# Optimization experiments

Measured on AMD Instinct MI355X. Metric: run time of the kernel, lower is better.

The kernel has to match this reference:

```python
import jax, jax.numpy as jnp
import numpy as np

B, H, W, C = 128, 8, 32, 512
RNN = 512; EMB = 512; ATT = 512
VOCAB = 110          # vocab_size -> classes = VOCAB + 1
MAXLEN = 30          # loop runs MAXLEN + 1 steps


def setup_inputs() -> dict:
    key = jax.random.key(0)
    ks = jax.random.split(key, 16)
    w = lambda i, shape: jax.random.normal(ks[i], shape, jnp.float32) * 0.02
    return {
        "features": jax.random.normal(ks[0], (B, H, W, C), jnp.float32),
        "holistic": jax.random.normal(ks[1], (B, RNN), jnp.float32),
        "gt": jax.random.randint(ks[2], (B, MAXLEN + 1), 0, VOCAB + 1),
        "embed_W": w(3, (VOCAB + 1, EMB)),
        "k0": w(4, (EMB, 4 * RNN)), "rk0": w(5, (RNN, 4 * RNN)), "b0": jnp.zeros((4 * RNN,), jnp.float32),
        "k1": w(6, (RNN, 4 * RNN)), "rk1": w(7, (RNN, 4 * RNN)), "b1": jnp.zeros((4 * RNN,), jnp.float32),
        "Wh": w(8, (RNN, ATT)),                       # 1x1 conv on (B,1,1,RNN) == dense
        "Wf": w(9, (3, 3, C, ATT)), "bf": jnp.zeros((ATT,), jnp.float32),
        "wa": w(10, (ATT, 1)),                        # 1x1 conv -> scalar attention logit
        "out_W": w(11, (2 * RNN, VOCAB + 1)), "out_b": jnp.zeros((VOCAB + 1,), jnp.float32),
    }


def _lstm(x, h, c, k, rk, b):
    # Keras LSTMCell: gates order i, f, g(cell), o
    z = x @ k + h @ rk + b
    i, f, g, o = jnp.split(z, 4, axis=-1)
    c2 = jax.nn.sigmoid(f) * c + jax.nn.sigmoid(i) * jnp.tanh(g)
    h2 = jax.nn.sigmoid(o) * jnp.tanh(c2)
    return h2, c2


def reference(features, holistic, gt, embed_W, k0, rk0, b0, k1, rk1, b1,
              Wh, Wf, bf, wa, out_W, out_b):
    Bb, Hh, Ww, Cc = features.shape
    # features_projector (3x3 conv, SAME) is timestep-invariant: precompute once
    fproj = jax.lax.conv_general_dilated(
        features, Wf, (1, 1), "SAME",
        dimension_numbers=("NHWC", "HWIO", "NHWC")) + bf          # (B,H,W,ATT)

    zeros = jnp.zeros((Bb, RNN), features.dtype)
    # prime stacked LSTM with holistic vector (zero initial state)
    h0, c0 = _lstm(holistic, zeros, zeros, k0, rk0, b0)
    h1, c1 = _lstm(h0, zeros, zeros, k1, rk1, b1)

    # teacher forcing: step 0 uses SOS token = vocab_size+1 (out-of-range -> zero one-hot),
    # step t>0 uses gt[:, t-1]
    sos = jnp.full((1, Bb), VOCAB + 1, gt.dtype)
    symbols = jnp.concatenate([sos, gt[:, :MAXLEN].T], axis=0)     # (T, B), T = MAXLEN+1

    def step(carry, sym):
        h0, c0, h1, c1 = carry
        x = jax.nn.one_hot(sym, VOCAB + 1, dtype=features.dtype) @ embed_W   # (B, EMB)
        h0, c0 = _lstm(x, h0, c0, k0, rk0, b0)
        h1, c1 = _lstm(h0, h1, c1, k1, rk1, b1)
        # attention over conv feature map
        hp = h1 @ Wh                                               # (B, ATT)
        proj = jnp.tanh(fproj + hp[:, None, None, :])              # (B,H,W,ATT)
        att = (proj @ wa).reshape(Bb, Hh * Ww)                     # (B, H*W)
        att = jax.nn.softmax(att, axis=-1).reshape(Bb, Hh, Ww, 1)
        glimpse = jnp.sum(features * att, axis=(1, 2))             # (B, C)
        logits = jnp.concatenate([h1, glimpse], axis=-1) @ out_W + out_b
        return (h0, c0, h1, c1), logits

    _, logits = jax.lax.scan(step, (h0, c0, h1, c1), symbols)      # (T, B, VOCAB+1)
    return jnp.transpose(logits, (1, 0, 2))                        # (B, T, VOCAB+1)
```

## Files before the change

### kernel.cpp

```cpp
#include <hip/hip_runtime.h>


typedef __bf16 bf16;
typedef bf16 bf16x8 __attribute__((ext_vector_type(8)));
typedef float f32x4 __attribute__((ext_vector_type(4)));

#define MFMA16(a, b, c) __builtin_amdgcn_mfma_f32_16x16x32_bf16((a), (b), (c), 0, 0, 0)

__device__ __forceinline__ float b2f(unsigned short u) {
    return __uint_as_float(((unsigned int)u) << 16);
}
__device__ __forceinline__ unsigned short f2b(float f) {
    unsigned int x = __float_as_uint(f);
    unsigned int r = (x + 0x7fffu + ((x >> 16) & 1u)) >> 16;
    return (unsigned short)r;
}
__device__ __forceinline__ float exp2_raw(float x) {
    float r;
    asm("v_exp_f32 %0, %1" : "=v"(r) : "v"(x));
    return r;
}
__device__ __forceinline__ float tanh_fast(float x) {
    const float e = exp2_raw(2.885390082f * x);
    return 1.0f - 2.0f * __builtin_amdgcn_rcpf(e + 1.0f);
}
__device__ __forceinline__ float sig_fast(float x) {
    return __builtin_amdgcn_rcpf(1.0f + exp2_raw(-1.44269504f * x));
}
__device__ __forceinline__ void gl16(const ushort* g, ushort* l) {
    __builtin_amdgcn_global_load_lds(
        (const __attribute__((address_space(1))) void*)g,
        (__attribute__((address_space(3))) void*)l, 16, 0, 0);
}

__global__ void detect_dtype(const void* __restrict__ feat, int* __restrict__ flag) {
    if (threadIdx.x == 0 && blockIdx.x == 0) {
        const ushort* u = (const ushort*)feat;
        int cnt = 0;
        for (int i = 0; i < 128; i += 2) {
            const int e = (u[i] >> 7) & 0xFF;
            if (e >= 96 && e <= 150) ++cnt;
        }
        *flag = (cnt >= 40) ? 0 : 1;
    }
}

__global__ __launch_bounds__(256) void cvt_bf16(
    const void* __restrict__ src, ushort* __restrict__ dst, int n,
    const int* __restrict__ flag) {
    const int i = blockIdx.x * 256 + threadIdx.x;
    if (i >= n) return;
    if (*flag) dst[i] = f2b(((const float*)src)[i]);
    else       dst[i] = ((const ushort*)src)[i];
}

__global__ __launch_bounds__(256) void cvt_f32(
    const void* __restrict__ src, float* __restrict__ dst, int n,
    const int* __restrict__ flag) {
    const int i = blockIdx.x * 256 + threadIdx.x;
    if (i >= n) return;
    if (*flag) dst[i] = ((const float*)src)[i];
    else       dst[i] = b2f(((const ushort*)src)[i]);
}

__global__ __launch_bounds__(256) void build_featpad(
    const void* __restrict__ feat, ushort* __restrict__ featPad,
    const int* __restrict__ flag) {
    const int i = blockIdx.x * 256 + threadIdx.x;
    if (i >= 128 * 10 * 34 * 512) return;
    const int c = i & 511;
    const int xy = i >> 9;
    const int x = xy % 34;
    const int t2 = xy / 34;
    const int y = t2 % 10;
    const int b = t2 / 10;
    ushort v = 0;
    if (y >= 1 && y <= 8 && x >= 1 && x <= 32) {
        const size_t si = ((size_t)((b * 8 + y - 1) * 32 + (x - 1)) << 9) + c;
        v = *flag ? f2b(((const float*)feat)[si]) : ((const ushort*)feat)[si];
    }
    featPad[i] = v;
}

__global__ __launch_bounds__(256) void transpose_any(
    const void* __restrict__ in, ushort* __restrict__ out, int R, int C,
    const int* __restrict__ flag) {
    __shared__ float s[32][33];
    const int f32 = *flag;
    const int nbc = C >> 5;
    const int rb = blockIdx.x / nbc, cb = blockIdx.x % nbc;
    const int tx = threadIdx.x & 31, ty = threadIdx.x >> 5;
#pragma unroll
    for (int k = 0; k < 4; ++k) {
        const size_t idx = (size_t)(rb * 32 + ty + k * 8) * C + cb * 32 + tx;
        s[ty + k * 8][tx] = f32 ? ((const float*)in)[idx] : b2f(((const ushort*)in)[idx]);
    }
    __syncthreads();
#pragma unroll
    for (int k = 0; k < 4; ++k)
        out[(size_t)(cb * 32 + ty + k * 8) * R + rb * 32 + tx] = f2b(s[tx][ty + k * 8]);
}

__global__ __launch_bounds__(256) void woT_build(
    const float* __restrict__ outWf, ushort* __restrict__ WoTpad) {
    const int i = blockIdx.x * 256 + threadIdx.x;
    if (i >= 131072) return;
    const int v = i >> 10, k = i & 1023;
    WoTpad[i] = (v < 111) ? f2b(outWf[k * 111 + v]) : (ushort)0;
}

__global__ __launch_bounds__(256) void conv_fproj(
    const ushort* __restrict__ featPad, const ushort* __restrict__ WfT,
    const float* __restrict__ bff, ushort* __restrict__ fproj) {
    __shared__ __align__(16) ushort As[128 * 64];
    __shared__ __align__(16) ushort Bs[128 * 64];
    const int tid = threadIdx.x;
    const int nb = blockIdx.x >> 8;
    const int rb = blockIdx.x & 255;
    const int b = rb >> 1, p0 = (rb & 1) << 7;
    const int w = tid >> 6, lane = tid & 63, l15 = lane & 15, q = lane >> 4;
    const int wr = (w >> 1) << 6, wc = (w & 1) << 6;
    const int chunkoff = (((lane & 7) ^ (lane >> 3)) << 3);
    int aoff[4], boff[4];
#pragma unroll
    for (int i = 0; i < 4; ++i) {
        const int r = w * 32 + (lane >> 3) + i * 8;
        const int p = p0 + r;
        const int yy = p >> 5, xx = p & 31;
        aoff[i] = (((b * 10 + yy) * 34 + xx) << 9) + chunkoff;
        boff[i] = (nb * 128 + r) * 4608 + chunkoff;
    }
    const int swa = l15 & 7;
    f32x4 acc[4][4] = {};
    for (int kb = 0; kb < 72; ++kb) {
        const int tap = kb >> 3;
        const int dy = tap / 3, dx = tap - dy * 3;
        const int koffA = ((dy * 34 + dx) << 9) + ((kb & 7) << 6);
        const int koffB = kb * 64;
        __syncthreads();
#pragma unroll
        for (int i = 0; i < 4; ++i) {
            gl16(featPad + aoff[i] + koffA, &As[(w * 32 + i * 8) * 64]);
            gl16(WfT + boff[i] + koffB, &Bs[(w * 32 + i * 8) * 64]);
        }
        __syncthreads();
#pragma unroll
        for (int ks = 0; ks < 64; ks += 32) {
            const int cq = (ks >> 3) + q;
            const int col = ((cq ^ swa) << 3);
            bf16x8 af[4], bfr[4];
#pragma unroll
            for (int i = 0; i < 4; ++i) af[i] = *(const bf16x8*)&As[(wr + i * 16 + l15) * 64 + col];
#pragma unroll
            for (int j = 0; j < 4; ++j) bfr[j] = *(const bf16x8*)&Bs[(wc + j * 16 + l15) * 64 + col];
#pragma unroll
            for (int i = 0; i < 4; ++i)
#pragma unroll
                for (int j = 0; j < 4; ++j)
                    acc[i][j] = MFMA16(af[i], bfr[j], acc[i][j]);
        }
    }
    const int rowbase = rb * 128 + wr, colbase = nb * 128 + wc;
#pragma unroll
    for (int i = 0; i < 4; ++i)
#pragma unroll
        for (int j = 0; j < 4; ++j)
#pragma unroll
            for (int rr = 0; rr < 4; ++rr) {
                const int row = rowbase + i * 16 + q * 4 + rr;
                const int col = colbase + j * 16 + l15;
                fproj[(size_t)row * 512 + col] = f2b(acc[i][j][rr] + bff[col]);
            }
}

__global__ __launch_bounds__(256) void gemm_bt(
    const ushort* __restrict__ A, const ushort* __restrict__ BT,
    float* __restrict__ C, int M, int N, int K, int lda) {
    __shared__ __align__(16) bf16 As[128][72];
    __shared__ __align__(16) bf16 Bs[128][72];
    const int tid = threadIdx.x;
    const int nnb = N >> 7;
    const int rb = blockIdx.x / nnb, nb = blockIdx.x % nnb;
    const int ar = tid >> 1, ah = (tid & 1) << 5;
    const int w = tid >> 6, lane = tid & 63, l15 = lane & 15, q = lane >> 4;
    const int wr = (w >> 1) << 6, wc = (w & 1) << 6;
    const int r_glob = rb * 128 + ar;
    const bool aval = (r_glob < M);
    const int r_ld = aval ? r_glob : 0;
    f32x4 acc[4][4] = {};
    const int nkb = K >> 6;
    for (int kb = 0; kb < nkb; ++kb) {
        const uint4 z4 = {0u, 0u, 0u, 0u};
        const uint4* asrc = (const uint4*)(A + (size_t)r_ld * lda + kb * 64 + ah);
        uint4 a0 = asrc[0], a1 = asrc[1], a2 = asrc[2], a3 = asrc[3];
        if (!aval) { a0 = z4; a1 = z4; a2 = z4; a3 = z4; }
        const uint4* bsrc = (const uint4*)(BT + (size_t)(nb * 128 + ar) * K + kb * 64 + ah);
        uint4 b0v = bsrc[0], b1v = bsrc[1], b2v = bsrc[2], b3v = bsrc[3];
        __syncthreads();
        *(uint4*)&As[ar][ah] = a0;
        *(uint4*)&As[ar][ah + 8] = a1;
        *(uint4*)&As[ar][ah + 16] = a2;
        *(uint4*)&As[ar][ah + 24] = a3;
        *(uint4*)&Bs[ar][ah] = b0v;
        *(uint4*)&Bs[ar][ah + 8] = b1v;
        *(uint4*)&Bs[ar][ah + 16] = b2v;
        *(uint4*)&Bs[ar][ah + 24] = b3v;
        __syncthreads();
#pragma unroll
        for (int ks = 0; ks < 64; ks += 32) {
            bf16x8 af[4], bfr[4];
#pragma unroll
            for (int i = 0; i < 4; ++i) af[i] = *(const bf16x8*)&As[wr + i * 16 + l15][ks + q * 8];
#pragma unroll
            for (int j = 0; j < 4; ++j) bfr[j] = *(const bf16x8*)&Bs[wc + j * 16 + l15][ks + q * 8];
#pragma unroll
            for (int i = 0; i < 4; ++i)
#pragma unroll
                for (int j = 0; j < 4; ++j)
                    acc[i][j] = MFMA16(af[i], bfr[j], acc[i][j]);
        }
    }
#pragma unroll
    for (int i = 0; i < 4; ++i)
#pragma unroll
        for (int j = 0; j < 4; ++j)
#pragma unroll
            for (int rr = 0; rr < 4; ++rr) {
                const int row = rb * 128 + wr + i * 16 + q * 4 + rr;
                const int col = nb * 128 + wc + j * 16 + l15;
                if (row < M) C[(size_t)row * N + col] = acc[i][j][rr];
            }
}

__global__ __launch_bounds__(256) void lstm_stage(
    int t,
    const ushort* __restrict__ holistic, const int* __restrict__ gt,
    const float* __restrict__ b0f, const float* __restrict__ b1f,
    const ushort* __restrict__ k0T, const ushort* __restrict__ rk0T,
    const ushort* __restrict__ k1T, const ushort* __restrict__ rk1T,
    const float* __restrict__ E0,
    ushort* h0b0, ushort* h0b1, ushort* h1b0, ushort* h1b1,
    float* c0buf, float* c1buf, ushort* HG) {
    const int part = blockIdx.x >> 7;
    const int bi = blockIdx.x & 127;
    const ushort *A1 = nullptr, *A2 = nullptr, *B1 = nullptr, *B2 = nullptr;
    const float* bias = nullptr;
    ushort *hout = nullptr, *hout2 = nullptr;
    float* cbuf = nullptr;
    bool useC = false, useE = false;
    if (part == 0) {
        if (!(t == -2 || (t >= 0 && t <= 30))) return;
        bias = b0f; cbuf = c0buf;
        if (t == -2) { A1 = holistic; B1 = k0T; hout = h0b1; }
        else {
            A1 = ((t + 1) & 1) ? h0b1 : h0b0;
            B1 = rk0T;
            hout = (t & 1) ? h0b1 : h0b0;
            useC = true; useE = true;
        }
    } else {
        if (!(t == -1 || (t >= 1 && t <= 31))) return;
        bias = b1f; cbuf = c1buf;
        if (t == -1) { A1 = h0b1; B1 = k1T; hout = h1b1; }
        else {
            const int s = t - 1;
            A1 = (s & 1) ? h0b1 : h0b0;
            A2 = ((s + 1) & 1) ? h1b1 : h1b0;
            B1 = k1T; B2 = rk1T;
            hout = (s & 1) ? h1b1 : h1b0;
            hout2 = HG + (size_t)s * 131072;
            useC = true;
        }
    }
    const int m0 = (bi >> 5) << 5;
    const int cc0 = (bi & 31) << 4;
    const int tid = threadIdx.x;
    const int w = tid >> 6, lane = tid & 63, l15 = lane & 15, q = lane >> 4;
    __shared__ __align__(16) ushort As1[32 * 520];
    __shared__ __align__(16) ushort As2[32 * 520];
    __shared__ float zs[4][32][17];
#pragma unroll
    for (int it = 0; it < 8; ++it) {
        const int idx = tid + it * 256;
        const int row = idx >> 6, chv = idx & 63;
        *(uint4*)&As1[row * 520 + chv * 8] =
            *(const uint4*)(A1 + (size_t)(m0 + row) * 512 + chv * 8);
    }
    if (A2) {
#pragma unroll
        for (int it = 0; it < 8; ++it) {
            const int idx = tid + it * 256;
            const int row = idx >> 6, chv = idx & 63;
            *(uint4*)&As2[row * 520 + chv * 8] =
                *(const uint4*)(A2 + (size_t)(m0 + row) * 512 + chv * 8);
        }
    }
    __syncthreads();
    const int nkb = A2 ? 16 : 8;
    const size_t brow = (size_t)(w * 512 + cc0 + l15) * 512 + q * 8;
    auto bp = [&](int kb) -> const ushort* {
        const ushort* base = (kb < 8) ? B1 : B2;
        return base + brow + (kb & 7) * 64;
    };
    bf16x8 b0a = *(const bf16x8*)bp(0), b1a = *(const bf16x8*)(bp(0) + 32);
    bf16x8 b0b = *(const bf16x8*)bp(1), b1b = *(const bf16x8*)(bp(1) + 32);
    bf16x8 b0c = *(const bf16x8*)bp(2), b1c = *(const bf16x8*)(bp(2) + 32);
    f32x4 acc0 = {}, acc1 = {};
    for (int kb = 0; kb < nkb; ++kb) {
        const bf16x8 p0 = b0a, p1 = b1a;
        b0a = b0b; b1a = b1b; b0b = b0c; b1b = b1c;
        if (kb + 3 < nkb) {
            b0c = *(const bf16x8*)bp(kb + 3);
            b1c = *(const bf16x8*)(bp(kb + 3) + 32);
        }
        const ushort* asrc = (kb < 8) ? As1 : As2;
        const int kk = (kb & 7) * 64 + q * 8;
        bf16x8 a00 = *(const bf16x8*)&asrc[l15 * 520 + kk];
        bf16x8 a10 = *(const bf16x8*)&asrc[(16 + l15) * 520 + kk];
        bf16x8 a01 = *(const bf16x8*)&asrc[l15 * 520 + kk + 32];
        bf16x8 a11 = *(const bf16x8*)&asrc[(16 + l15) * 520 + kk + 32];
        acc0 = MFMA16(a00, p0, acc0);
        acc1 = MFMA16(a10, p0, acc1);
        acc0 = MFMA16(a01, p1, acc0);
        acc1 = MFMA16(a11, p1, acc1);
    }
#pragma unroll
    for (int rr = 0; rr < 4; ++rr) {
        zs[w][q * 4 + rr][l15] = acc0[rr];
        zs[w][16 + q * 4 + rr][l15] = acc1[rr];
    }
    __syncthreads();
#pragma unroll
    for (int it = 0; it < 2; ++it) {
        const int e = tid + it * 256;
        const int mm = e >> 4, cc = e & 15;
        const int brow2 = m0 + mm, col = cc0 + cc;
        float zi = zs[0][mm][cc] + bias[col];
        float zf = zs[1][mm][cc] + bias[512 + col];
        float zg = zs[2][mm][cc] + bias[1024 + col];
        float zo = zs[3][mm][cc] + bias[1536 + col];
        if (useE) {
            const int s = (t == 0) ? 111 : gt[brow2 * 31 + t - 1];
            if (s >= 0 && s < 111) {
                const float* er = E0 + (size_t)s * 2048;
                zi += er[col]; zf += er[512 + col]; zg += er[1024 + col]; zo += er[1536 + col];
            }
        }
        const float cp = useC ? cbuf[brow2 * 512 + col] : 0.0f;
        const float c2 = sig_fast(zf) * cp + sig_fast(zi) * tanh_fast(zg);
        const float h = sig_fast(zo) * tanh_fast(c2);
        cbuf[brow2 * 512 + col] = c2;
        hout[brow2 * 512 + col] = f2b(h);
        if (hout2) hout2[brow2 * 1024 + col] = f2b(h);
    }
}

__global__ __launch_bounds__(256) void att_logits(
    const ushort* __restrict__ fproj, const float* __restrict__ HP,
    const float* __restrict__ waf, float* __restrict__ attL) {
    __shared__ float hpS[16][512];
    __shared__ float waS[512];
    __shared__ float accS[128][17];
    const int tid = threadIdx.x;
    const int b = blockIdx.x >> 2, ph = (blockIdx.x >> 1) & 1, th = blockIdx.x & 1;
    const int t0 = th << 4, tc = th ? 15 : 16;
    const int pl = tid & 127, ch = tid >> 7;
    const int p = ph * 128 + pl;
    for (int i = tid; i < 16 * 512; i += 256) {
        const int tt = i >> 9, c = i & 511;
        hpS[tt][c] = (tt < tc) ? 2.885390082f * HP[((size_t)(t0 + tt) * 128 + b) * 512 + c] : 0.0f;
    }
    waS[tid] = -2.0f * waf[tid];
    if (tid < 256) waS[256 + tid] = -2.0f * waf[256 + tid];
    __syncthreads();
    float sumW = 0.f;
    {
        const float* wh = &waS[ch * 256];
        for (int c4 = 0; c4 < 64; ++c4) {
            const float4 wv = *(const float4*)&wh[c4 * 4];
            sumW += wv.x + wv.y + wv.z + wv.w;
        }
        sumW *= -0.5f;
    }
    float acc[16];
#pragma unroll
    for (int tt = 0; tt < 16; ++tt) acc[tt] = 0.f;
    const ushort* frow = fproj + (size_t)(b * 256 + p) * 512 + ch * 256;
    for (int c8 = 0; c8 < 32; ++c8) {
        const int cc = ch * 256 + c8 * 8;
        const uint4 fv = *(const uint4*)(frow + c8 * 8);
        float f[8];
        f[0] = b2f((unsigned short)(fv.x & 0xffff)); f[1] = b2f((unsigned short)(fv.x >> 16));
        f[2] = b2f((unsigned short)(fv.y & 0xffff)); f[3] = b2f((unsigned short)(fv.y >> 16));
        f[4] = b2f((unsigned short)(fv.z & 0xffff)); f[5] = b2f((unsigned short)(fv.z >> 16));
        f[6] = b2f((unsigned short)(fv.w & 0xffff)); f[7] = b2f((unsigned short)(fv.w >> 16));
#pragma unroll
        for (int j = 0; j < 8; ++j) f[j] *= 2.885390082f;
        const float4 w0 = *(const float4*)&waS[cc];
        const float4 w1 = *(const float4*)&waS[cc + 4];
#pragma unroll
        for (int tt = 0; tt < 16; ++tt) {
            const float4 h0 = *(const float4*)&hpS[tt][cc];
            const float4 h1 = *(const float4*)&hpS[tt][cc + 4];
            float s = acc[tt];
            s = fmaf(__builtin_amdgcn_rcpf(exp2_raw(f[0] + h0.x) + 1.0f), w0.x, s);
            s = fmaf(__builtin_amdgcn_rcpf(exp2_raw(f[1] + h0.y) + 1.0f), w0.y, s);
            s = fmaf(__builtin_amdgcn_rcpf(exp2_raw(f[2] + h0.z) + 1.0f), w0.z, s);
            s = fmaf(__builtin_amdgcn_rcpf(exp2_raw(f[3] + h0.w) + 1.0f), w0.w, s);
            s = fmaf(__builtin_amdgcn_rcpf(exp2_raw(f[4] + h1.x) + 1.0f), w1.x, s);
            s = fmaf(__builtin_amdgcn_rcpf(exp2_raw(f[5] + h1.y) + 1.0f), w1.y, s);
            s = fmaf(__builtin_amdgcn_rcpf(exp2_raw(f[6] + h1.z) + 1.0f), w1.z, s);
            s = fmaf(__builtin_amdgcn_rcpf(exp2_raw(f[7] + h1.w) + 1.0f), w1.w, s);
            acc[tt] = s;
        }
    }
    if (ch == 1) {
#pragma unroll
        for (int tt = 0; tt < 16; ++tt) accS[pl][tt] = acc[tt] + sumW;
    }
    __syncthreads();
    if (ch == 0) {
        for (int tt = 0; tt < tc; ++tt)
            attL[((size_t)(t0 + tt) * 128 + b) * 256 + p] = acc[tt] + sumW + accS[pl][tt];
    }
}

__global__ __launch_bounds__(256) void glimpse_kernel(
    const ushort* __restrict__ featPad, const float* __restrict__ attL,
    ushort* __restrict__ HG) {
    __shared__ __align__(16) float attT[256 * 36];
    const int tid = threadIdx.x;
    const int b = blockIdx.x >> 1, chh = blockIdx.x & 1;
    const int c0 = chh << 8;
    const int w = tid >> 6, lane = tid & 63;
    for (int i = tid; i < 31 * 256; i += 256) {
        const int tt = i >> 8, p = i & 255;
        attT[p * 36 + tt] = attL[((size_t)tt * 128 + b) * 256 + p];
    }
    __syncthreads();
    for (int tt = w; tt < 31; tt += 4) {
        float v0 = attT[lane * 36 + tt], v1 = attT[(lane + 64) * 36 + tt];
        float v2 = attT[(lane + 128) * 36 + tt], v3 = attT[(lane + 192) * 36 + tt];
        float mx = fmaxf(fmaxf(v0, v1), fmaxf(v2, v3));
#pragma unroll
        for (int m = 1; m < 64; m <<= 1) mx = fmaxf(mx, __shfl_xor(mx, m));
        const float e0 = exp2_raw((v0 - mx) * 1.44269504f);
        const float e1 = exp2_raw((v1 - mx) * 1.44269504f);
        const float e2 = exp2_raw((v2 - mx) * 1.44269504f);
        const float e3 = exp2_raw((v3 - mx) * 1.44269504f);
        float s = e0 + e1 + e2 + e3;
#pragma unroll
        for (int m = 1; m < 64; m <<= 1) s += __shfl_xor(s, m);
        const float r = 1.0f / s;
        attT[lane * 36 + tt] = e0 * r;  attT[(lane + 64) * 36 + tt] = e1 * r;
        attT[(lane + 128) * 36 + tt] = e2 * r;  attT[(lane + 192) * 36 + tt] = e3 * r;
    }
    __syncthreads();
    float acc[31];
#pragma unroll
    for (int tt = 0; tt < 31; ++tt) acc[tt] = 0.f;
    for (int p = 0; p < 256; ++p) {
        const size_t fi = (((size_t)(b * 10 + (p >> 5) + 1) * 34 + (p & 31) + 1) << 9) + c0 + tid;
        const float fv = b2f(featPad[fi]);
        const float4 a0 = *(const float4*)&attT[p * 36];
        const float4 a1 = *(const float4*)&attT[p * 36 + 4];
        const float4 a2 = *(const float4*)&attT[p * 36 + 8];
        const float4 a3 = *(const float4*)&attT[p * 36 + 12];
        const float4 a4 = *(const float4*)&attT[p * 36 + 16];
        const float4 a5 = *(const float4*)&attT[p * 36 + 20];
        const float4 a6 = *(const float4*)&attT[p * 36 + 24];
        const float4 a7 = *(const float4*)&attT[p * 36 + 28];
        acc[0] = fmaf(fv, a0.x, acc[0]);   acc[1] = fmaf(fv, a0.y, acc[1]);
        acc[2] = fmaf(fv, a0.z, acc[2]);   acc[3] = fmaf(fv, a0.w, acc[3]);
        acc[4] = fmaf(fv, a1.x, acc[4]);   acc[5] = fmaf(fv, a1.y, acc[5]);
        acc[6] = fmaf(fv, a1.z, acc[6]);   acc[7] = fmaf(fv, a1.w, acc[7]);
        acc[8] = fmaf(fv, a2.x, acc[8]);   acc[9] = fmaf(fv, a2.y, acc[9]);
        acc[10] = fmaf(fv, a2.z, acc[10]); acc[11] = fmaf(fv, a2.w, acc[11]);
        acc[12] = fmaf(fv, a3.x, acc[12]); acc[13] = fmaf(fv, a3.y, acc[13]);
        acc[14] = fmaf(fv, a3.z, acc[14]); acc[15] = fmaf(fv, a3.w, acc[15]);
        acc[16] = fmaf(fv, a4.x, acc[16]); acc[17] = fmaf(fv, a4.y, acc[17]);
        acc[18] = fmaf(fv, a4.z, acc[18]); acc[19] = fmaf(fv, a4.w, acc[19]);
        acc[20] = fmaf(fv, a5.x, acc[20]); acc[21] = fmaf(fv, a5.y, acc[21]);
        acc[22] = fmaf(fv, a5.z, acc[22]); acc[23] = fmaf(fv, a5.w, acc[23]);
        acc[24] = fmaf(fv, a6.x, acc[24]); acc[25] = fmaf(fv, a6.y, acc[25]);
        acc[26] = fmaf(fv, a6.z, acc[26]); acc[27] = fmaf(fv, a6.w, acc[27]);
        acc[28] = fmaf(fv, a7.x, acc[28]); acc[29] = fmaf(fv, a7.y, acc[29]);
        acc[30] = fmaf(fv, a7.z, acc[30]);
    }
#pragma unroll
    for (int tt = 0; tt < 31; ++tt)
        HG[((size_t)tt * 128 + b) * 1024 + 512 + c0 + tid] = f2b(acc[tt]);
}

__global__ __launch_bounds__(256) void logits_store(
    const float* __restrict__ C, const float* __restrict__ outBf,
    void* __restrict__ out, const int* __restrict__ flag) {
    const int i = blockIdx.x * 256 + threadIdx.x;
    if (i >= 3968 * 111) return;
    const int r = i / 111, v = i - r * 111;
    const int tt = r >> 7, b = r & 127;
    const float a = C[(size_t)r * 128 + v] + outBf[v];
    const size_t oi = ((size_t)b * 31 + tt) * 111 + v;
    if (*flag) ((float*)out)[oi] = a;
    else       ((ushort*)out)[oi] = f2b(a);
}

extern "C" void kernel_launch(void* const* d_in, const int* in_sizes, int n_in,
                              void* d_out, int out_size, void* d_ws, size_t ws_size,
                              hipStream_t stream) {
    (void)in_sizes; (void)n_in; (void)out_size;
    const void* features = d_in[0];
    const void* holistic = d_in[1];
    const int*  gt       = (const int*)d_in[2];
    const void* embed_W  = d_in[3];
    const void* k0 = d_in[4];
    const void* rk0 = d_in[5];
    const void* b0 = d_in[6];
    const void* k1 = d_in[7];
    const void* rk1 = d_in[8];
    const void* b1 = d_in[9];
    const void* Wh = d_in[10];
    const void* Wf = d_in[11];
    const void* bfv = d_in[12];
    const void* wa = d_in[13];
    const void* outW = d_in[14];
    const void* outB = d_in[15];

    char* ws = (char*)d_ws;
    size_t off = 0;
    auto take = [&](size_t bytes) -> char* {
        char* p = ws + off;
        off += (bytes + 255) & ~(size_t)255;
        return p;
    };
    int*    flag    = (int*)take(256);
    ushort* featPad = (ushort*)take(128ull * 10 * 34 * 512 * 2);
    ushort* holB  = (ushort*)take(65536ull * 2);
    ushort* embB  = (ushort*)take(56832ull * 2);
    float*  b0f   = (float*)take(2048ull * 4);
    float*  b1f   = (float*)take(2048ull * 4);
    float*  bff   = (float*)take(512ull * 4);
    float*  waf   = (float*)take(512ull * 4);
    float*  outBf = (float*)take(111ull * 4);
    float*  outWf = (float*)take(113664ull * 4);
    ushort* fproj = (ushort*)take(32768ull * 512 * 2);
    ushort* WfT   = (ushort*)take(4608ull * 512 * 2);
    ushort* k0T   = (ushort*)take(2048ull * 512 * 2);
    ushort* rk0T  = (ushort*)take(2048ull * 512 * 2);
    ushort* k1T   = (ushort*)take(2048ull * 512 * 2);
    ushort* rk1T  = (ushort*)take(2048ull * 512 * 2);
    ushort* WhT   = (ushort*)take(512ull * 512 * 2);
    float*  E0    = (float*)take(111ull * 2048 * 4);
    ushort* h0b0  = (ushort*)take(128ull * 512 * 2);
    ushort* h0b1  = (ushort*)take(128ull * 512 * 2);
    ushort* h1b0  = (ushort*)take(128ull * 512 * 2);
    ushort* h1b1  = (ushort*)take(128ull * 512 * 2);
    float*  c0buf = (float*)take(128ull * 512 * 4);
    float*  c1buf = (float*)take(128ull * 512 * 4);
    ushort* HG    = (ushort*)take(3968ull * 1024 * 2);
    float*  HP    = (float*)take(3968ull * 512 * 4);
    float*  attL  = (float*)take(31ull * 128 * 256 * 4);
    float*  Cout   = (float*)attL;
    ushort* WoTpad = (ushort*)((char*)attL + 3968ull * 128 * 4);
    if (off > ws_size) return;

    detect_dtype<<<dim3(1), dim3(64), 0, stream>>>(features, flag);
    build_featpad<<<dim3(87040), dim3(256), 0, stream>>>(features, featPad, flag);
    cvt_bf16<<<dim3(256), dim3(256), 0, stream>>>(holistic, holB, 65536, flag);
    cvt_bf16<<<dim3(222), dim3(256), 0, stream>>>(embed_W, embB, 56832, flag);
    cvt_f32<<<dim3(8), dim3(256), 0, stream>>>(b0, b0f, 2048, flag);
    cvt_f32<<<dim3(8), dim3(256), 0, stream>>>(b1, b1f, 2048, flag);
    cvt_f32<<<dim3(2), dim3(256), 0, stream>>>(bfv, bff, 512, flag);
    cvt_f32<<<dim3(2), dim3(256), 0, stream>>>(wa, waf, 512, flag);
    cvt_f32<<<dim3(1), dim3(256), 0, stream>>>(outB, outBf, 111, flag);
    cvt_f32<<<dim3(444), dim3(256), 0, stream>>>(outW, outWf, 113664, flag);
    transpose_any<<<dim3(16 * 64), dim3(256), 0, stream>>>(k0, k0T, 512, 2048, flag);
    transpose_any<<<dim3(16 * 64), dim3(256), 0, stream>>>(rk0, rk0T, 512, 2048, flag);
    transpose_any<<<dim3(16 * 64), dim3(256), 0, stream>>>(k1, k1T, 512, 2048, flag);
    transpose_any<<<dim3(16 * 64), dim3(256), 0, stream>>>(rk1, rk1T, 512, 2048, flag);
    transpose_any<<<dim3(16 * 16), dim3(256), 0, stream>>>(Wh, WhT, 512, 512, flag);
    transpose_any<<<dim3(144 * 16), dim3(256), 0, stream>>>(Wf, WfT, 4608, 512, flag);
    conv_fproj<<<dim3(1024), dim3(256), 0, stream>>>(featPad, WfT, bff, fproj);
    gemm_bt<<<dim3(16), dim3(256), 0, stream>>>(embB, k0T, E0, 111, 2048, 512, 512);
    for (int t = -2; t <= 31; ++t)
        lstm_stage<<<dim3(256), dim3(256), 0, stream>>>(t, holB, gt, b0f, b1f,
            k0T, rk0T, k1T, rk1T, E0, h0b0, h0b1, h1b0, h1b1, c0buf, c1buf, HG);
    gemm_bt<<<dim3(31 * 4), dim3(256), 0, stream>>>(HG, WhT, HP, 3968, 512, 512, 1024);
    att_logits<<<dim3(512), dim3(256), 0, stream>>>(fproj, HP, waf, attL);
    glimpse_kernel<<<dim3(256), dim3(256), 0, stream>>>(featPad, attL, HG);
    woT_build<<<dim3(512), dim3(256), 0, stream>>>(outWf, WoTpad);
    gemm_bt<<<dim3(31), dim3(256), 0, stream>>>(HG, WoTpad, Cout, 3968, 128, 1024, 1024);
    logits_store<<<dim3(1721), dim3(256), 0, stream>>>(Cout, outBf, d_out, flag);
}
```

Before: 933.4 us.

## Fuse conv projection and LSTM steps into one persistent kernel with grid barriers

Replaces the 34 per-timestep LSTM launches with one persistent kernel whose 256 LSTM blocks loop over timesteps and sync through atomic counters acting as grid barriers. The same launch also carries the 1024 conv_fproj blocks, so the timestep-invariant conv can run alongside the serial LSTM chain instead of before it. This removes launch overhead and overlaps the conv with the recurrence. It relies on all 256 LSTM blocks being co-resident and risks deadlock or slowdown if conv blocks take the CUs first. Sharing one large shared-memory buffer may also lower occupancy for the conv blocks.

```diff
diff --git a/kernel.cpp b/kernel.cpp
--- a/kernel.cpp
+++ b/kernel.cpp
@@ -43,6 +43,10 @@
         }
         *flag = (cnt >= 40) ? 0 : 1;
     }
+}
+
+__global__ void zero_cnt(int* __restrict__ cnt) {
+    if (threadIdx.x < 64) cnt[threadIdx.x] = 0;
 }
 
 __global__ __launch_bounds__(256) void cvt_bf16(
@@ -107,70 +111,6 @@
     if (i >= 131072) return;
     const int v = i >> 10, k = i & 1023;
     WoTpad[i] = (v < 111) ? f2b(outWf[k * 111 + v]) : (ushort)0;
-}
-
-__global__ __launch_bounds__(256) void conv_fproj(
-    const ushort* __restrict__ featPad, const ushort* __restrict__ WfT,
-    const float* __restrict__ bff, ushort* __restrict__ fproj) {
-    __shared__ __align__(16) ushort As[128 * 64];
-    __shared__ __align__(16) ushort Bs[128 * 64];
-    const int tid = threadIdx.x;
-    const int nb = blockIdx.x >> 8;
-    const int rb = blockIdx.x & 255;
-    const int b = rb >> 1, p0 = (rb & 1) << 7;
-    const int w = tid >> 6, lane = tid & 63, l15 = lane & 15, q = lane >> 4;
-    const int wr = (w >> 1) << 6, wc = (w & 1) << 6;
-    const int chunkoff = (((lane & 7) ^ (lane >> 3)) << 3);
-    int aoff[4], boff[4];
-#pragma unroll
-    for (int i = 0; i < 4; ++i) {
-        const int r = w * 32 + (lane >> 3) + i * 8;
-        const int p = p0 + r;
-        const int yy = p >> 5, xx = p & 31;
-        aoff[i] = (((b * 10 + yy) * 34 + xx) << 9) + chunkoff;
-        boff[i] = (nb * 128 + r) * 4608 + chunkoff;
-    }
-    const int swa = l15 & 7;
-    f32x4 acc[4][4] = {};
-    for (int kb = 0; kb < 72; ++kb) {
-        const int tap = kb >> 3;
-        const int dy = tap / 3, dx = tap - dy * 3;
-        const int koffA = ((dy * 34 + dx) << 9) + ((kb & 7) << 6);
-        const int koffB = kb * 64;
-        __syncthreads();
-#pragma unroll
-        for (int i = 0; i < 4; ++i) {
-            gl16(featPad + aoff[i] + koffA, &As[(w * 32 + i * 8) * 64]);
-            gl16(WfT + boff[i] + koffB, &Bs[(w * 32 + i * 8) * 64]);
-        }
-        __syncthreads();
-#pragma unroll
-        for (int ks = 0; ks < 64; ks += 32) {
-            const int cq = (ks >> 3) + q;
-            const int col = ((cq ^ swa) << 3);
-            bf16x8 af[4], bfr[4];
-#pragma unroll
-            for (int i = 0; i < 4; ++i) af[i] = *(const bf16x8*)&As[(wr + i * 16 + l15) * 64 + col];
-#pragma unroll
-            for (int j = 0; j < 4; ++j) bfr[j] = *(const bf16x8*)&Bs[(wc + j * 16 + l15) * 64 + col];
-#pragma unroll
-            for (int i = 0; i < 4; ++i)
-#pragma unroll
-                for (int j = 0; j < 4; ++j)
-                    acc[i][j] = MFMA16(af[i], bfr[j], acc[i][j]);
-        }
-    }
-    const int rowbase = rb * 128 + wr, colbase = nb * 128 + wc;
-#pragma unroll
-    for (int i = 0; i < 4; ++i)
-#pragma unroll
-        for (int j = 0; j < 4; ++j)
-#pragma unroll
-            for (int rr = 0; rr < 4; ++rr) {
-                const int row = rowbase + i * 16 + q * 4 + rr;
-                const int col = colbase + j * 16 + l15;
-                fproj[(size_t)row * 512 + col] = f2b(acc[i][j][rr] + bff[col]);
-            }
 }
 
 __global__ __launch_bounds__(256) void gemm_bt(
@@ -232,126 +172,213 @@
             }
 }
 
-__global__ __launch_bounds__(256) void lstm_stage(
-    int t,
+__global__ __launch_bounds__(256) void conv_lstm_mega(
+    const ushort* __restrict__ featPad, const ushort* __restrict__ WfT,
+    const float* __restrict__ bff, ushort* __restrict__ fproj,
     const ushort* __restrict__ holistic, const int* __restrict__ gt,
     const float* __restrict__ b0f, const float* __restrict__ b1f,
     const ushort* __restrict__ k0T, const ushort* __restrict__ rk0T,
     const ushort* __restrict__ k1T, const ushort* __restrict__ rk1T,
     const float* __restrict__ E0,
     ushort* h0b0, ushort* h0b1, ushort* h1b0, ushort* h1b1,
-    float* c0buf, float* c1buf, ushort* HG) {
+    float* c0buf, float* c1buf, ushort* HG, int* cnt) {
+    __shared__ __align__(16) ushort smem[37632];
+    const int tid = threadIdx.x;
+    const int w = tid >> 6, lane = tid & 63, l15 = lane & 15, q = lane >> 4;
+
+    if (blockIdx.x >= 256) {
+        ushort* As = smem;
+        ushort* Bs = smem + 8192;
+        const int cidx = blockIdx.x - 256;
+        const int nb = cidx >> 8;
+        const int rb = cidx & 255;
+        const int b = rb >> 1, p0 = (rb & 1) << 7;
+        const int wr = (w >> 1) << 6, wc = (w & 1) << 6;
+        const int chunkoff = (((lane & 7) ^ (lane >> 3)) << 3);
+        int aoff[4], boff[4];
+#pragma unroll
+        for (int i = 0; i < 4; ++i) {
+            const int r = w * 32 + (lane >> 3) + i * 8;
+            const int p = p0 + r;
+            const int yy = p >> 5, xx = p & 31;
+            aoff[i] = (((b * 10 + yy) * 34 + xx) << 9) + chunkoff;
+            boff[i] = (nb * 128 + r) * 4608 + chunkoff;
+        }
+        const int swa = l15 & 7;
+        f32x4 acc[4][4] = {};
+        for (int kb = 0; kb < 72; ++kb) {
+            const int tap = kb >> 3;
+            const int dy = tap / 3, dx = tap - dy * 3;
+            const int koffA = ((dy * 34 + dx) << 9) + ((kb & 7) << 6);
+            const int koffB = kb * 64;
+            __syncthreads();
+#pragma unroll
+            for (int i = 0; i < 4; ++i) {
+                gl16(featPad + aoff[i] + koffA, &As[(w * 32 + i * 8) * 64]);
+                gl16(WfT + boff[i] + koffB, &Bs[(w * 32 + i * 8) * 64]);
+            }
+            __syncthreads();
+#pragma unroll
+            for (int ks = 0; ks < 64; ks += 32) {
+                const int cq = (ks >> 3) + q;
+                const int col = ((cq ^ swa) << 3);
+                bf16x8 af[4], bfr[4];
+#pragma unroll
+                for (int i = 0; i < 4; ++i) af[i] = *(const bf16x8*)&As[(wr + i * 16 + l15) * 64 + col];
+#pragma unroll
+                for (int j = 0; j < 4; ++j) bfr[j] = *(const bf16x8*)&Bs[(wc + j * 16 + l15) * 64 + col];
+#pragma unroll
+                for (int i = 0; i < 4; ++i)
+#pragma unroll
+                    for (int j = 0; j < 4; ++j)
+                        acc[i][j] = MFMA16(af[i], bfr[j], acc[i][j]);
+            }
+        }
+        const int rowbase = rb * 128 + wr, colbase = nb * 128 + wc;
+#pragma unroll
+        for (int i = 0; i < 4; ++i)
+#pragma unroll
+            for (int j = 0; j < 4; ++j)
+#pragma unroll
+                for (int rr = 0; rr < 4; ++rr) {
+                    const int row = rowbase + i * 16 + q * 4 + rr;
+                    const int col = colbase + j * 16 + l15;
+                    fproj[(size_t)row * 512 + col] = f2b(acc[i][j][rr] + bff[col]);
+                }
+        return;
+    }
+
+    ushort* As1 = smem;
+    ushort* As2 = smem + 16640;
+    float*  zsf = (float*)(smem + 33280);
     const int part = blockIdx.x >> 7;
     const int bi = blockIdx.x & 127;
-    const ushort *A1 = nullptr, *A2 = nullptr, *B1 = nullptr, *B2 = nullptr;
-    const float* bias = nullptr;
-    ushort *hout = nullptr, *hout2 = nullptr;
-    float* cbuf = nullptr;
-    bool useC = false, useE = false;
-    if (part == 0) {
-        if (!(t == -2 || (t >= 0 && t <= 30))) return;
-        bias = b0f; cbuf = c0buf;
-        if (t == -2) { A1 = holistic; B1 = k0T; hout = h0b1; }
-        else {
-            A1 = ((t + 1) & 1) ? h0b1 : h0b0;
-            B1 = rk0T;
-            hout = (t & 1) ? h0b1 : h0b0;
-            useC = true; useE = true;
-        }
-    } else {
-        if (!(t == -1 || (t >= 1 && t <= 31))) return;
-        bias = b1f; cbuf = c1buf;
-        if (t == -1) { A1 = h0b1; B1 = k1T; hout = h1b1; }
-        else {
-            const int s = t - 1;
-            A1 = (s & 1) ? h0b1 : h0b0;
-            A2 = ((s + 1) & 1) ? h1b1 : h1b0;
-            B1 = k1T; B2 = rk1T;
-            hout = (s & 1) ? h1b1 : h1b0;
-            hout2 = HG + (size_t)s * 131072;
-            useC = true;
-        }
-    }
     const int m0 = (bi >> 5) << 5;
     const int cc0 = (bi & 31) << 4;
-    const int tid = threadIdx.x;
-    const int w = tid >> 6, lane = tid & 63, l15 = lane & 15, q = lane >> 4;
-    __shared__ __align__(16) ushort As1[32 * 520];
-    __shared__ __align__(16) ushort As2[32 * 520];
-    __shared__ float zs[4][32][17];
-#pragma unroll
-    for (int it = 0; it < 8; ++it) {
-        const int idx = tid + it * 256;
-        const int row = idx >> 6, chv = idx & 63;
-        *(uint4*)&As1[row * 520 + chv * 8] =
-            *(const uint4*)(A1 + (size_t)(m0 + row) * 512 + chv * 8);
-    }
-    if (A2) {
-#pragma unroll
-        for (int it = 0; it < 8; ++it) {
-            const int idx = tid + it * 256;
-            const int row = idx >> 6, chv = idx & 63;
-            *(uint4*)&As2[row * 520 + chv * 8] =
-                *(const uint4*)(A2 + (size_t)(m0 + row) * 512 + chv * 8);
-        }
-    }
-    __syncthreads();
-    const int nkb = A2 ? 16 : 8;
-    const size_t brow = (size_t)(w * 512 + cc0 + l15) * 512 + q * 8;
-    auto bp = [&](int kb) -> const ushort* {
-        const ushort* base = (kb < 8) ? B1 : B2;
-        return base + brow + (kb & 7) * 64;
-    };
-    bf16x8 b0a = *(const bf16x8*)bp(0), b1a = *(const bf16x8*)(bp(0) + 32);
-    bf16x8 b0b = *(const bf16x8*)bp(1), b1b = *(const bf16x8*)(bp(1) + 32);
-    bf16x8 b0c = *(const bf16x8*)bp(2), b1c = *(const bf16x8*)(bp(2) + 32);
-    f32x4 acc0 = {}, acc1 = {};
-    for (int kb = 0; kb < nkb; ++kb) {
-        const bf16x8 p0 = b0a, p1 = b1a;
-        b0a = b0b; b1a = b1b; b0b = b0c; b1b = b1c;
-        if (kb + 3 < nkb) {
-            b0c = *(const bf16x8*)bp(kb + 3);
-            b1c = *(const bf16x8*)(bp(kb + 3) + 32);
-        }
-        const ushort* asrc = (kb < 8) ? As1 : As2;
-        const int kk = (kb & 7) * 64 + q * 8;
-        bf16x8 a00 = *(const bf16x8*)&asrc[l15 * 520 + kk];
-        bf16x8 a10 = *(const bf16x8*)&asrc[(16 + l15) * 520 + kk];
-        bf16x8 a01 = *(const bf16x8*)&asrc[l15 * 520 + kk + 32];
-        bf16x8 a11 = *(const bf16x8*)&asrc[(16 + l15) * 520 + kk + 32];
-        acc0 = MFMA16(a00, p0, acc0);
-        acc1 = MFMA16(a10, p0, acc1);
-        acc0 = MFMA16(a01, p1, acc0);
-        acc1 = MFMA16(a11, p1, acc1);
-    }
-#pragma unroll
-    for (int rr = 0; rr < 4; ++rr) {
-        zs[w][q * 4 + rr][l15] = acc0[rr];
-        zs[w][16 + q * 4 + rr][l15] = acc1[rr];
-    }
-    __syncthreads();
-#pragma unroll
-    for (int it = 0; it < 2; ++it) {
-        const int e = tid + it * 256;
-        const int mm = e >> 4, cc = e & 15;
-        const int brow2 = m0 + mm, col = cc0 + cc;
-        float zi = zs[0][mm][cc] + bias[col];
-        float zf = zs[1][mm][cc] + bias[512 + col];
-        float zg = zs[2][mm][cc] + bias[1024 + col];
-        float zo = zs[3][mm][cc] + bias[1536 + col];
-        if (useE) {
-            const int s = (t == 0) ? 111 : gt[brow2 * 31 + t - 1];
-            if (s >= 0 && s < 111) {
-                const float* er = E0 + (size_t)s * 2048;
-                zi += er[col]; zf += er[512 + col]; zg += er[1024 + col]; zo += er[1536 + col];
-            }
-        }
-        const float cp = useC ? cbuf[brow2 * 512 + col] : 0.0f;
-        const float c2 = sig_fast(zf) * cp + sig_fast(zi) * tanh_fast(zg);
-        const float h = sig_fast(zo) * tanh_fast(c2);
-        cbuf[brow2 * 512 + col] = c2;
-        hout[brow2 * 512 + col] = f2b(h);
-        if (hout2) hout2[brow2 * 1024 + col] = f2b(h);
+
+    for (int t = -2; t <= 31; ++t) {
+        const int k = t + 2;
+        if (k > 0) {
+            if (tid == 0) {
+                while (__hip_atomic_load(&cnt[k - 1], __ATOMIC_RELAXED,
+                                         __HIP_MEMORY_SCOPE_AGENT) < 256)
+                    __builtin_amdgcn_s_sleep(1);
+            }
+            __syncthreads();
+            __threadfence();
+        }
+        const ushort *A1 = nullptr, *A2 = nullptr, *B1 = nullptr, *B2 = nullptr;
+        const float* bias = nullptr;
+        ushort *hout = nullptr, *hout2 = nullptr;
+        float* cbuf = nullptr;
+        bool useC = false, useE = false, active = false;
+        if (part == 0) {
+            if (t == -2 || (t >= 0 && t <= 30)) {
+                active = true; bias = b0f; cbuf = c0buf;
+                if (t == -2) { A1 = holistic; B1 = k0T; hout = h0b1; }
+                else {
+                    A1 = ((t + 1) & 1) ? h0b1 : h0b0;
+                    B1 = rk0T;
+                    hout = (t & 1) ? h0b1 : h0b0;
+                    useC = true; useE = true;
+                }
+            }
+        } else {
+            if (t == -1 || (t >= 1 && t <= 31)) {
+                active = true; bias = b1f; cbuf = c1buf;
+                if (t == -1) { A1 = h0b1; B1 = k1T; hout = h1b1; }
+                else {
+                    const int s = t - 1;
+                    A1 = (s & 1) ? h0b1 : h0b0;
+                    A2 = ((s + 1) & 1) ? h1b1 : h1b0;
+                    B1 = k1T; B2 = rk1T;
+                    hout = (s & 1) ? h1b1 : h1b0;
+                    hout2 = HG + (size_t)s * 131072;
+                    useC = true;
+                }
+            }
+        }
+        if (active) {
+#pragma unroll
+            for (int it = 0; it < 8; ++it) {
+                const int idx = tid + it * 256;
+                const int row = idx >> 6, chv = idx & 63;
+                *(uint4*)&As1[row * 520 + chv * 8] =
+                    *(const uint4*)(A1 + (size_t)(m0 + row) * 512 + chv * 8);
+            }
+            if (A2) {
+#pragma unroll
+                for (int it = 0; it < 8; ++it) {
+                    const int idx = tid + it * 256;
+                    const int row = idx >> 6, chv = idx & 63;
+                    *(uint4*)&As2[row * 520 + chv * 8] =
+                        *(const uint4*)(A2 + (size_t)(m0 + row) * 512 + chv * 8);
+                }
+            }
+            __syncthreads();
+            const int nkb = A2 ? 16 : 8;
+            const size_t brow = (size_t)(w * 512 + cc0 + l15) * 512 + q * 8;
+            auto bp = [&](int kb) -> const ushort* {
+                const ushort* base = (kb < 8) ? B1 : B2;
+                return base + brow + (kb & 7) * 64;
+            };
+            bf16x8 b0a = *(const bf16x8*)bp(0), b1a = *(const bf16x8*)(bp(0) + 32);
+            bf16x8 b0b = *(const bf16x8*)bp(1), b1b = *(const bf16x8*)(bp(1) + 32);
+            bf16x8 b0c = *(const bf16x8*)bp(2), b1c = *(const bf16x8*)(bp(2) + 32);
+            f32x4 acc0 = {}, acc1 = {};
+            for (int kb = 0; kb < nkb; ++kb) {
+                const bf16x8 p0 = b0a, p1 = b1a;
+                b0a = b0b; b1a = b1b; b0b = b0c; b1b = b1c;
+                if (kb + 3 < nkb) {
+                    b0c = *(const bf16x8*)bp(kb + 3);
+                    b1c = *(const bf16x8*)(bp(kb + 3) + 32);
+                }
+                const ushort* asrc = (kb < 8) ? As1 : As2;
+                const int kk = (kb & 7) * 64 + q * 8;
+                bf16x8 a00 = *(const bf16x8*)&asrc[l15 * 520 + kk];
+                bf16x8 a10 = *(const bf16x8*)&asrc[(16 + l15) * 520 + kk];
+                bf16x8 a01 = *(const bf16x8*)&asrc[l15 * 520 + kk + 32];
+                bf16x8 a11 = *(const bf16x8*)&asrc[(16 + l15) * 520 + kk + 32];
+                acc0 = MFMA16(a00, p0, acc0);
+                acc1 = MFMA16(a10, p0, acc1);
+                acc0 = MFMA16(a01, p1, acc0);
+                acc1 = MFMA16(a11, p1, acc1);
+            }
+#pragma unroll
+            for (int rr = 0; rr < 4; ++rr) {
+                zsf[w * 544 + (q * 4 + rr) * 17 + l15] = acc0[rr];
+                zsf[w * 544 + (16 + q * 4 + rr) * 17 + l15] = acc1[rr];
+            }
+            __syncthreads();
+#pragma unroll
+            for (int it = 0; it < 2; ++it) {
+                const int e = tid + it * 256;
+                const int mm = e >> 4, cc = e & 15;
+                const int brow2 = m0 + mm, col = cc0 + cc;
+                float zi = zsf[0 * 544 + mm * 17 + cc] + bias[col];
+                float zf = zsf[1 * 544 + mm * 17 + cc] + bias[512 + col];
+                float zg = zsf[2 * 544 + mm * 17 + cc] + bias[1024 + col];
+                float zo = zsf[3 * 544 + mm * 17 + cc] + bias[1536 + col];
+                if (useE) {
+                    const int s = (t == 0) ? 111 : gt[brow2 * 31 + t - 1];
+                    if (s >= 0 && s < 111) {
+                        const float* er = E0 + (size_t)s * 2048;
+                        zi += er[col]; zf += er[512 + col]; zg += er[1024 + col]; zo += er[1536 + col];
+                    }
+                }
+                const float cp = useC ? cbuf[brow2 * 512 + col] : 0.0f;
+                const float c2 = sig_fast(zf) * cp + sig_fast(zi) * tanh_fast(zg);
+                const float h = sig_fast(zo) * tanh_fast(c2);
+                cbuf[brow2 * 512 + col] = c2;
+                hout[brow2 * 512 + col] = f2b(h);
+                if (hout2) hout2[brow2 * 1024 + col] = f2b(h);
+            }
+        }
+        __syncthreads();
+        __threadfence();
+        if (tid == 0)
+            __hip_atomic_fetch_add(&cnt[k], 1, __ATOMIC_RELEASE,
+                                   __HIP_MEMORY_SCOPE_AGENT);
     }
 }
 
@@ -534,6 +561,7 @@
         return p;
     };
     int*    flag    = (int*)take(256);
+    int*    cnt     = (int*)take(256);
     ushort* featPad = (ushort*)take(128ull * 10 * 34 * 512 * 2);
     ushort* holB  = (ushort*)take(65536ull * 2);
     ushort* embB  = (ushort*)take(56832ull * 2);
@@ -565,6 +593,7 @@
     if (off > ws_size) return;
 
     detect_dtype<<<dim3(1), dim3(64), 0, stream>>>(features, flag);
+    zero_cnt<<<dim3(1), dim3(64), 0, stream>>>(cnt);
     build_featpad<<<dim3(87040), dim3(256), 0, stream>>>(features, featPad, flag);
     cvt_bf16<<<dim3(256), dim3(256), 0, stream>>>(holistic, holB, 65536, flag);
     cvt_bf16<<<dim3(222), dim3(256), 0, stream>>>(embed_W, embB, 56832, flag);
@@ -580,11 +609,11 @@
     transpose_any<<<dim3(16 * 64), dim3(256), 0, stream>>>(rk1, rk1T, 512, 2048, flag);
     transpose_any<<<dim3(16 * 16), dim3(256), 0, stream>>>(Wh, WhT, 512, 512, flag);
     transpose_any<<<dim3(144 * 16), dim3(256), 0, stream>>>(Wf, WfT, 4608, 512, flag);
-    conv_fproj<<<dim3(1024), dim3(256), 0, stream>>>(featPad, WfT, bff, fproj);
     gemm_bt<<<dim3(16), dim3(256), 0, stream>>>(embB, k0T, E0, 111, 2048, 512, 512);
-    for (int t = -2; t <= 31; ++t)
-        lstm_stage<<<dim3(256), dim3(256), 0, stream>>>(t, holB, gt, b0f, b1f,
-            k0T, rk0T, k1T, rk1T, E0, h0b0, h0b1, h1b0, h1b1, c0buf, c1buf, HG);
+    conv_lstm_mega<<<dim3(1280), dim3(256), 0, stream>>>(
+        featPad, WfT, bff, fproj,
+        holB, gt, b0f, b1f, k0T, rk0T, k1T, rk1T, E0,
+        h0b0, h0b1, h1b0, h1b1, c0buf, c1buf, HG, cnt);
     gemm_bt<<<dim3(31 * 4), dim3(256), 0, stream>>>(HG, WhT, HP, 3968, 512, 512, 1024);
     att_logits<<<dim3(512), dim3(256), 0, stream>>>(fproj, HP, waf, attL);
     glimpse_kernel<<<dim3(256), dim3(256), 0, stream>>>(featPad, attL, HG);
```

Result: slower. 2.990 ms (+220.4%).
